# Performance work log

Measured on AMD Instinct MI355X. Metric: run time of the kernel, lower is better.

The kernel has to match this reference:

```python
import jax, jax.numpy as jnp
import numpy as np

N_NODES = 100000
N_EDGES = 1600000
N_GRAPHS = 256
F_NODE, F_EDGE, HID, OUT = 64, 16, 128, 128
BN_SCALE = 1.0 / np.sqrt(1.0 + 1e-5)  # BatchNorm eval with running mean 0, var 1


def setup_inputs() -> dict:
    key = jax.random.key(0)
    ks = iter(jax.random.split(key, 64))
    inp = {}
    inp["x"] = jax.random.normal(next(ks), (N_NODES, F_NODE), dtype=jnp.float32)
    inp["edge_attr"] = jax.random.normal(next(ks), (N_EDGES, F_EDGE), dtype=jnp.float32)
    inp["edge_index"] = jax.random.randint(next(ks), (2, N_EDGES), 0, N_NODES)
    inp["batch"] = jnp.sort(jax.random.randint(next(ks), (N_NODES,), 0, N_GRAPHS))

    def p(shape, scale):
        return (jax.random.normal(next(ks), shape, dtype=jnp.float32) * scale)

    in_dims = [F_NODE, HID, HID]
    for i, d in enumerate(in_dims):
        inp[f"el_w{i}"] = p((F_EDGE, d), F_EDGE ** -0.5)
        inp[f"el_b{i}"] = jnp.zeros((d,), jnp.float32)
        inp[f"c{i}_w1"] = p((d, HID), d ** -0.5)
        inp[f"c{i}_b1"] = jnp.zeros((HID,), jnp.float32)
        inp[f"c{i}_g"] = jnp.ones((HID,), jnp.float32)
        inp[f"c{i}_bt"] = jnp.zeros((HID,), jnp.float32)
        inp[f"c{i}_w2"] = p((HID, HID), HID ** -0.5)
        inp[f"c{i}_b2"] = jnp.zeros((HID,), jnp.float32)
    inp["o_w1"] = p((HID, OUT), HID ** -0.5)
    inp["o_b1"] = jnp.zeros((OUT,), jnp.float32)
    inp["o_w2"] = p((OUT, OUT), OUT ** -0.5)
    inp["o_b2"] = jnp.zeros((OUT,), jnp.float32)
    return inp


def reference(x, edge_attr,
              el_w0, el_b0, c0_w1, c0_b1, c0_g, c0_bt, c0_w2, c0_b2,
              el_w1, el_b1, c1_w1, c1_b1, c1_g, c1_bt, c1_w2, c1_b2,
              el_w2, el_b2, c2_w1, c2_b1, c2_g, c2_bt, c2_w2, c2_b2,
              o_w1, o_b1, o_w2, o_b2,
              edge_index, batch):
    src, dst = edge_index[0], edge_index[1]
    n = x.shape[0]
    layers = [
        (el_w0, el_b0, c0_w1, c0_b1, c0_g, c0_bt, c0_w2, c0_b2),
        (el_w1, el_b1, c1_w1, c1_b1, c1_g, c1_bt, c1_w2, c1_b2),
        (el_w2, el_b2, c2_w1, c2_b1, c2_g, c2_bt, c2_w2, c2_b2),
    ]
    h = x
    for (ew, eb, w1, b1, g, bt, w2, b2) in layers:
        ea = edge_attr @ ew + eb                              # [E, d]
        msg = jax.nn.relu(h[src] + ea)                        # GINEConv message
        agg = jax.ops.segment_sum(msg, dst, num_segments=n)   # scatter-sum to targets
        hh = h + agg                                          # (1+eps)*x + aggr, eps=0
        hh = hh @ w1 + b1                                     # MLP: Linear
        hh = g * (hh * BN_SCALE) + bt                         # BatchNorm1d (eval)
        hh = jax.nn.relu(hh)
        hh = hh @ w2 + b2                                     # MLP: Linear
        h = jax.nn.relu(hh)                                   # dropout(p=0, eval) + act
    s = jax.ops.segment_sum(h, batch, num_segments=N_GRAPHS)
    cnt = jax.ops.segment_sum(jnp.ones((n,), h.dtype), batch, num_segments=N_GRAPHS)
    pooled = s / jnp.maximum(cnt, 1.0)[:, None]               # scatter-mean pooling
    out = jax.nn.relu(pooled @ o_w1 + o_b1) @ o_w2 + o_b2     # out_lin
    return out
```

## Files before the change

### kernel.cpp

```cpp
#include <hip/hip_runtime.h>
#include <hip/hip_fp16.h>
#include <cstdint>
#include <cstddef>

#define N_NODES_C  100000
#define N_EDGES_C  1600000
#define N_GRAPHS_C 256
#define HID_C      128
#define BN_SCALE_C 0.9999950000374997f

#define SCAN_B 1024
#define SCAN_NB ((N_NODES_C + SCAN_B - 1) / SCAN_B)

typedef _Float16 h8 __attribute__((ext_vector_type(8)));
typedef _Float16 h4 __attribute__((ext_vector_type(4)));
typedef float    f4 __attribute__((ext_vector_type(4)));

struct __align__(16) H8 { __half2 v[4]; };
struct __align__(8)  Hq { __half2 a, b; };

__global__ __launch_bounds__(256) void hist_kernel(
    const int* __restrict__ dst, int* __restrict__ counts, int n_edges)
{
    int e = blockIdx.x * 256 + threadIdx.x;
    if (e < n_edges) atomicAdd(&counts[dst[e]], 1);
}

__global__ __launch_bounds__(SCAN_B) void scan1_kernel(
    const int* __restrict__ counts, int* __restrict__ incl,
    int* __restrict__ blocksums, int n)
{
    __shared__ int sdata[SCAN_B];
    const int lid = threadIdx.x;
    const int i = blockIdx.x * SCAN_B + lid;
    sdata[lid] = (i < n) ? counts[i] : 0;
    __syncthreads();
#pragma unroll
    for (int off = 1; off < SCAN_B; off <<= 1) {
        int t = (lid >= off) ? sdata[lid - off] : 0;
        __syncthreads();
        sdata[lid] += t;
        __syncthreads();
    }
    if (i < n) incl[i] = sdata[lid];
    if (lid == SCAN_B - 1) blocksums[blockIdx.x] = sdata[lid];
}

__global__ void scan2_kernel(const int* __restrict__ blocksums,
                             int* __restrict__ blockoffs, int nb)
{
    if (threadIdx.x == 0 && blockIdx.x == 0) {
        int off = 0;
        for (int b = 0; b < nb; ++b) { blockoffs[b] = off; off += blocksums[b]; }
    }
}

__global__ __launch_bounds__(SCAN_B) void scan3_kernel(
    int* __restrict__ incl, const int* __restrict__ blockoffs, int n)
{
    const int i = blockIdx.x * SCAN_B + threadIdx.x;
    if (i < n) incl[i] += blockoffs[blockIdx.x];
}

__global__ __launch_bounds__(256) void initrows_kernel(
    const int* __restrict__ incl, const int* __restrict__ counts,
    int* __restrict__ rowstart, int* __restrict__ cursor, int n)
{
    const int i = blockIdx.x * 256 + threadIdx.x;
    if (i < n) {
        const int rs = incl[i] - counts[i];
        rowstart[i] = rs;
        cursor[i]   = rs;
    }
}

__global__ __launch_bounds__(256) void scatter_kernel(
    const int* __restrict__ src, const int* __restrict__ dst,
    int* __restrict__ cursor, int* __restrict__ perm_src,
    int* __restrict__ perm_eid, int n_edges)
{
    const int e = blockIdx.x * 256 + threadIdx.x;
    if (e < n_edges) {
        const int pos = atomicAdd(&cursor[dst[e]], 1);
        perm_src[pos] = src[e];
        perm_eid[pos] = e;
    }
}

__global__ __launch_bounds__(256) void permute_ea_f16_kernel(
    const float* __restrict__ edge_attr, const int* __restrict__ perm_eid,
    __half* __restrict__ ea_f16, int n_edges)
{
    const int j = blockIdx.x * 256 + threadIdx.x;
    if (j >= n_edges) return;
    const int eid = perm_eid[j];
    const float4* p = (const float4*)(edge_attr + (size_t)eid * 16);
    const float4 q0 = p[0], q1 = p[1], q2 = p[2], q3 = p[3];
    H8 a, b;
    a.v[0] = __floats2half2_rn(q0.x, q0.y);
    a.v[1] = __floats2half2_rn(q0.z, q0.w);
    a.v[2] = __floats2half2_rn(q1.x, q1.y);
    a.v[3] = __floats2half2_rn(q1.z, q1.w);
    b.v[0] = __floats2half2_rn(q2.x, q2.y);
    b.v[1] = __floats2half2_rn(q2.z, q2.w);
    b.v[2] = __floats2half2_rn(q3.x, q3.y);
    b.v[3] = __floats2half2_rn(q3.z, q3.w);
    H8* o = (H8*)(ea_f16 + (size_t)j * 16);
    o[0] = a;
    o[1] = b;
}

__global__ __launch_bounds__(256) void cast_f16_kernel(
    const float* __restrict__ in, _Float16* __restrict__ out, int n4)
{
    const int i = blockIdx.x * 256 + threadIdx.x;
    if (i >= n4) return;
    const float4 v = ((const float4*)in)[i];
    h4 o; o[0] = (_Float16)v.x; o[1] = (_Float16)v.y;
    o[2] = (_Float16)v.z; o[3] = (_Float16)v.w;
    *(h4*)(out + (size_t)i * 4) = o;
}

__global__ __launch_bounds__(256) void transpose_w_kernel(
    const float* __restrict__ w, _Float16* __restrict__ wt, int K, int N)
{
    const int i = blockIdx.x * 256 + threadIdx.x;
    if (i >= K * N) return;
    const int n = i / K;
    const int k = i - n * K;
    wt[(size_t)n * K + k] = (_Float16)w[(size_t)k * N + n];
}

__device__ __forceinline__ float4 eamlp_f16(const H8* __restrict__ p,
                                            const __half2 (*ew2)[4],
                                            const float4 ebv)
{
    const H8 a = p[0], b = p[1];
    __half2 c0 = {0.f, 0.f}, c1 = {0.f, 0.f}, c2 = {0.f, 0.f}, c3 = {0.f, 0.f};
#pragma unroll
    for (int k2 = 0; k2 < 4; ++k2) {
        c0 = __hfma2(a.v[k2], ew2[k2][0], c0);
        c1 = __hfma2(a.v[k2], ew2[k2][1], c1);
        c2 = __hfma2(a.v[k2], ew2[k2][2], c2);
        c3 = __hfma2(a.v[k2], ew2[k2][3], c3);
    }
#pragma unroll
    for (int k2 = 0; k2 < 4; ++k2) {
        c0 = __hfma2(b.v[k2], ew2[4 + k2][0], c0);
        c1 = __hfma2(b.v[k2], ew2[4 + k2][1], c1);
        c2 = __hfma2(b.v[k2], ew2[4 + k2][2], c2);
        c3 = __hfma2(b.v[k2], ew2[4 + k2][3], c3);
    }
    float4 m;
    m.x = ebv.x + __low2float(c0) + __high2float(c0);
    m.y = ebv.y + __low2float(c1) + __high2float(c1);
    m.z = ebv.z + __low2float(c2) + __high2float(c2);
    m.w = ebv.w + __low2float(c3) + __high2float(c3);
    return m;
}

template<int DIN>
__global__ __launch_bounds__(256) void gine_agg_kernel(
    const __half* __restrict__ h16, const __half* __restrict__ ea_f16,
    const int* __restrict__ perm_src,
    const int* __restrict__ rowstart, const int* __restrict__ rowend,
    const float* __restrict__ ew, const float* __restrict__ eb,
    float* __restrict__ agg, int n_nodes)
{
    constexpr int NQ    = DIN / 4;
    constexpr int SLOTS = 256 / NQ;
    const int fq   = threadIdx.x & (NQ - 1);
    const int slot = threadIdx.x / NQ;
    const int v = blockIdx.x * SLOTS + slot;
    if (v >= n_nodes) return;

    __half2 ew2[8][4];
#pragma unroll
    for (int k2 = 0; k2 < 8; ++k2)
#pragma unroll
        for (int fi = 0; fi < 4; ++fi)
            ew2[k2][fi] = __floats2half2_rn(ew[(size_t)(2 * k2)     * DIN + fq * 4 + fi],
                                            ew[(size_t)(2 * k2 + 1) * DIN + fq * 4 + fi]);
    const float4 ebv = *(const float4*)(eb + fq * 4);

    const int s0 = rowstart[v];
    const int s1 = rowend[v];

    float4 acc = {0.f, 0.f, 0.f, 0.f};
    int j = s0;
    for (; j + 2 <= s1; j += 2) {
        const int sn0 = perm_src[j + 0];
        const int sn1 = perm_src[j + 1];
        const Hq hq0 = *(const Hq*)(h16 + (size_t)sn0 * DIN + fq * 4);
        const Hq hq1 = *(const Hq*)(h16 + (size_t)sn1 * DIN + fq * 4);
        const H8* p0 = (const H8*)(ea_f16 + (size_t)(j + 0) * 16);
        const H8* p1 = (const H8*)(ea_f16 + (size_t)(j + 1) * 16);
        const float4 m0 = eamlp_f16(p0, ew2, ebv);
        const float4 m1 = eamlp_f16(p1, ew2, ebv);
        const float2 l0 = __half22float2(hq0.a), u0 = __half22float2(hq0.b);
        const float2 l1 = __half22float2(hq1.a), u1 = __half22float2(hq1.b);
        acc.x += fmaxf(m0.x + l0.x, 0.f) + fmaxf(m1.x + l1.x, 0.f);
        acc.y += fmaxf(m0.y + l0.y, 0.f) + fmaxf(m1.y + l1.y, 0.f);
        acc.z += fmaxf(m0.z + u0.x, 0.f) + fmaxf(m1.z + u1.x, 0.f);
        acc.w += fmaxf(m0.w + u0.y, 0.f) + fmaxf(m1.w + u1.y, 0.f);
    }
    if (j < s1) {
        const int sn = perm_src[j];
        const Hq hq = *(const Hq*)(h16 + (size_t)sn * DIN + fq * 4);
        const H8* p = (const H8*)(ea_f16 + (size_t)j * 16);
        const float4 m = eamlp_f16(p, ew2, ebv);
        const float2 l = __half22float2(hq.a), u = __half22float2(hq.b);
        acc.x += fmaxf(m.x + l.x, 0.f);
        acc.y += fmaxf(m.y + l.y, 0.f);
        acc.z += fmaxf(m.z + u.x, 0.f);
        acc.w += fmaxf(m.w + u.y, 0.f);
    }
    *(float4*)(agg + (size_t)v * DIN + fq * 4) = acc;
}

template<int DIN>
__global__ __launch_bounds__(256) void node_mfma_kernel(
    const float* __restrict__ h, const float* __restrict__ agg,
    const _Float16* __restrict__ w1t, const float* __restrict__ b1,
    const float* __restrict__ gm, const float* __restrict__ bt,
    const _Float16* __restrict__ w2t, const float* __restrict__ b2,
    float* __restrict__ hout, _Float16* __restrict__ h16out, int n_tiles)
{
    constexpr int SXP = DIN + 8;
    constexpr int STP = HID_C + 8;
    __shared__ _Float16 s_x[4][16][SXP];
    __shared__ _Float16 s_t[4][16][STP];

    const int w    = threadIdx.x >> 6;
    const int lane = threadIdx.x & 63;
    int tile = blockIdx.x * 4 + w;
    if (tile >= n_tiles) tile = n_tiles - 1;
    const int node0 = tile * 16;

    constexpr int KQ = DIN / 4;
    for (int it = lane; it < 16 * KQ; it += 64) {
        const int ni = it / KQ;
        const int k4 = (it - ni * KQ) * 4;
        const float4 hv = *(const float4*)(h   + (size_t)(node0 + ni) * DIN + k4);
        const float4 av = *(const float4*)(agg + (size_t)(node0 + ni) * DIN + k4);
        h4 o;
        o[0] = (_Float16)(hv.x + av.x);
        o[1] = (_Float16)(hv.y + av.y);
        o[2] = (_Float16)(hv.z + av.z);
        o[3] = (_Float16)(hv.w + av.w);
        *(h4*)&s_x[w][ni][k4] = o;
    }
    __syncthreads();

    const int ln   = lane & 15;
    const int quad = lane >> 4;

#pragma unroll
    for (int nt = 0; nt < 8; ++nt) {
        const int col = nt * 16 + ln;
        const float bv = b1[col];
        f4 acc = {bv, bv, bv, bv};
#pragma unroll
        for (int ks = 0; ks < DIN / 32; ++ks) {
            const h8 af = *(const h8*)&s_x[w][ln][ks * 32 + quad * 8];
            const h8 bf = *(const h8*)(w1t + (size_t)col * DIN + ks * 32 + quad * 8);
            acc = __builtin_amdgcn_mfma_f32_16x16x32_f16(af, bf, acc, 0, 0, 0);
        }
        const float gv = gm[col], btv = bt[col];
#pragma unroll
        for (int r = 0; r < 4; ++r) {
            const float t = fmaxf(fmaf(acc[r] * BN_SCALE_C, gv, btv), 0.f);
            s_t[w][quad * 4 + r][col] = (_Float16)t;
        }
    }
    __syncthreads();

#pragma unroll
    for (int nt = 0; nt < 8; ++nt) {
        const int col = nt * 16 + ln;
        const float bv = b2[col];
        f4 acc = {bv, bv, bv, bv};
#pragma unroll
        for (int ks = 0; ks < HID_C / 32; ++ks) {
            const h8 af = *(const h8*)&s_t[w][ln][ks * 32 + quad * 8];
            const h8 bf = *(const h8*)(w2t + (size_t)col * HID_C + ks * 32 + quad * 8);
            acc = __builtin_amdgcn_mfma_f32_16x16x32_f16(af, bf, acc, 0, 0, 0);
        }
#pragma unroll
        for (int r = 0; r < 4; ++r) {
            const int node = node0 + quad * 4 + r;
            const float v = fmaxf(acc[r], 0.f);
            hout[(size_t)node * HID_C + col] = v;
            h16out[(size_t)node * HID_C + col] = (_Float16)v;
        }
    }
}

__global__ __launch_bounds__(256) void pool_kernel(
    const float* __restrict__ hfin, const int* __restrict__ batch,
    const float* __restrict__ w1, const float* __restrict__ b1,
    const float* __restrict__ w2, const float* __restrict__ b2,
    float* __restrict__ out, int n_nodes)
{
    const int gid = blockIdx.x;

    int lo = 0, hi = n_nodes;
    while (lo < hi) { int mid = (lo + hi) >> 1; if (batch[mid] < gid) lo = mid + 1; else hi = mid; }
    const int start = lo;
    hi = n_nodes;
    while (lo < hi) { int mid = (lo + hi) >> 1; if (batch[mid] < gid + 1) lo = mid + 1; else hi = mid; }
    const int end = lo;

    const int f = threadIdx.x & (HID_C - 1);
    const int half = threadIdx.x >> 7;

    float sum = 0.f;
    for (int n = start + half; n < end; n += 2)
        sum += hfin[(size_t)n * HID_C + f];

    __shared__ float s_sum[2][HID_C];
    __shared__ float s_p[HID_C];
    __shared__ float s_t[HID_C];
    s_sum[half][f] = sum;
    __syncthreads();

    if (threadIdx.x < HID_C) {
        const float cnt = (float)(end - start);
        s_p[f] = (s_sum[0][f] + s_sum[1][f]) / fmaxf(cnt, 1.f);
    }
    __syncthreads();

    if (threadIdx.x < HID_C) {
        float acc = b1[f];
        for (int k = 0; k < HID_C; ++k) acc = fmaf(s_p[k], w1[k * HID_C + f], acc);
        s_t[f] = fmaxf(acc, 0.f);
    }
    __syncthreads();

    if (threadIdx.x < HID_C) {
        float acc = b2[f];
        for (int k = 0; k < HID_C; ++k) acc = fmaf(s_t[k], w2[k * HID_C + f], acc);
        out[(size_t)gid * HID_C + f] = acc;
    }
}

extern "C" void kernel_launch(void* const* d_in, const int* in_sizes, int n_in,
                              void* d_out, int out_size, void* d_ws, size_t ws_size,
                              hipStream_t stream)
{
    const float* x         = (const float*)d_in[0];
    const float* edge_attr = (const float*)d_in[1];
    const int*   edge_index= (const int*)  d_in[2];
    const int*   batch     = (const int*)  d_in[3];
    const int*   src = edge_index;
    const int*   dst = edge_index + N_EDGES_C;

    const float* el_w[3] = {(const float*)d_in[4],  (const float*)d_in[12], (const float*)d_in[20]};
    const float* el_b[3] = {(const float*)d_in[5],  (const float*)d_in[13], (const float*)d_in[21]};
    const float* c_w1[3] = {(const float*)d_in[6],  (const float*)d_in[14], (const float*)d_in[22]};
    const float* c_b1[3] = {(const float*)d_in[7],  (const float*)d_in[15], (const float*)d_in[23]};
    const float* c_g [3] = {(const float*)d_in[8],  (const float*)d_in[16], (const float*)d_in[24]};
    const float* c_bt[3] = {(const float*)d_in[9],  (const float*)d_in[17], (const float*)d_in[25]};
    const float* c_w2[3] = {(const float*)d_in[10], (const float*)d_in[18], (const float*)d_in[26]};
    const float* c_b2[3] = {(const float*)d_in[11], (const float*)d_in[19], (const float*)d_in[27]};
    const float* o_w1 = (const float*)d_in[28];
    const float* o_b1 = (const float*)d_in[29];
    const float* o_w2 = (const float*)d_in[30];
    const float* o_b2 = (const float*)d_in[31];

    char* wsp = (char*)d_ws;
    size_t used = 0;
    auto alloc = [&](size_t bytes) { char* p = wsp + used; used += (bytes + 255) & ~(size_t)255; return p; };
    float* h        = (float*)alloc((size_t)N_NODES_C * HID_C * 4);
    float* agg      = (float*)alloc((size_t)N_NODES_C * HID_C * 4);
    int*   counts   = (int*)alloc((size_t)N_NODES_C * 4);
    int*   incl     = (int*)alloc((size_t)N_NODES_C * 4);
    int*   rowstart = (int*)alloc((size_t)N_NODES_C * 4);
    int*   cursor   = (int*)alloc((size_t)N_NODES_C * 4);
    int*   blocksums= (int*)alloc(128 * 4);
    int*   blockoffs= (int*)alloc(128 * 4);
    int*   perm_src = (int*)alloc((size_t)N_EDGES_C * 4);
    int*   perm_eid = (int*)alloc((size_t)N_EDGES_C * 4);
    __half*    ea_f16 = (__half*)alloc((size_t)N_EDGES_C * 16 * 2);
    _Float16*  h_f16  = (_Float16*)alloc((size_t)N_NODES_C * HID_C * 2);
    _Float16*  x_f16  = (_Float16*)alloc((size_t)N_NODES_C * 64 * 2);
    _Float16*  w1t[3], *w2t[3];
    for (int l = 0; l < 3; ++l) {
        w1t[l] = (_Float16*)alloc((size_t)HID_C * HID_C * 2);
        w2t[l] = (_Float16*)alloc((size_t)HID_C * HID_C * 2);
    }
    (void)ws_size;

    hipMemsetAsync(counts, 0, (size_t)N_NODES_C * 4, stream);
    hist_kernel<<<(N_EDGES_C + 255) / 256, 256, 0, stream>>>(dst, counts, N_EDGES_C);
    scan1_kernel<<<SCAN_NB, SCAN_B, 0, stream>>>(counts, incl, blocksums, N_NODES_C);
    scan2_kernel<<<1, 64, 0, stream>>>(blocksums, blockoffs, SCAN_NB);
    scan3_kernel<<<SCAN_NB, SCAN_B, 0, stream>>>(incl, blockoffs, N_NODES_C);
    initrows_kernel<<<(N_NODES_C + 255) / 256, 256, 0, stream>>>(incl, counts, rowstart,
                                                                 cursor, N_NODES_C);
    scatter_kernel<<<(N_EDGES_C + 255) / 256, 256, 0, stream>>>(src, dst, cursor,
                                                                perm_src, perm_eid, N_EDGES_C);
    permute_ea_f16_kernel<<<(N_EDGES_C + 255) / 256, 256, 0, stream>>>(
        edge_attr, perm_eid, ea_f16, N_EDGES_C);
    cast_f16_kernel<<<(N_NODES_C * 64 / 4 + 255) / 256, 256, 0, stream>>>(
        x, x_f16, N_NODES_C * 64 / 4);
    for (int l = 0; l < 3; ++l) {
        const int K1 = (l == 0) ? 64 : HID_C;
        transpose_w_kernel<<<(K1 * HID_C + 255) / 256, 256, 0, stream>>>(
            c_w1[l], w1t[l], K1, HID_C);
        transpose_w_kernel<<<(HID_C * HID_C + 255) / 256, 256, 0, stream>>>(
            c_w2[l], w2t[l], HID_C, HID_C);
    }

    const int n_tiles = N_NODES_C / 16;
    const int nb_node = (n_tiles + 3) / 4;

    for (int l = 0; l < 3; ++l) {
        if (l == 0) {
            gine_agg_kernel<64><<<(N_NODES_C + 15) / 16, 256, 0, stream>>>(
                (const __half*)x_f16, ea_f16, perm_src, rowstart, incl,
                el_w[0], el_b[0], agg, N_NODES_C);
            node_mfma_kernel<64><<<nb_node, 256, 0, stream>>>(
                x, agg, w1t[0], c_b1[0], c_g[0], c_bt[0], w2t[0], c_b2[0],
                h, h_f16, n_tiles);
        } else {
            gine_agg_kernel<128><<<(N_NODES_C + 7) / 8, 256, 0, stream>>>(
                (const __half*)h_f16, ea_f16, perm_src, rowstart, incl,
                el_w[l], el_b[l], agg, N_NODES_C);
            node_mfma_kernel<128><<<nb_node, 256, 0, stream>>>(
                h, agg, w1t[l], c_b1[l], c_g[l], c_bt[l], w2t[l], c_b2[l],
                h, h_f16, n_tiles);
        }
    }

    pool_kernel<<<N_GRAPHS_C, 256, 0, stream>>>(h, batch, o_w1, o_b1, o_w2, o_b2,
                                                (float*)d_out, N_NODES_C);
}
```

Before: 1.114 ms.

## Fuse edge aggregation with node MLP into one per-layer kernel

Merges the gather/aggregate kernel and the MFMA node MLP kernel into a single per-layer kernel. Each wavefront aggregates messages for its 16-node tile straight into shared memory, which removes the fp32 agg buffer round trip and the fp32 h reads. Hidden states now ping-pong between fp16 buffers, and only the last layer writes fp32. The edge MLP switches from packed half FMAs to fdot2 with fp32 accumulation. Blocks shrink to 128 threads with 2 tiles each, which may cost load balance and repeats the edge-weight register setup per wave.

```diff
diff --git a/kernel.cpp b/kernel.cpp
--- a/kernel.cpp
+++ b/kernel.cpp
@@ -12,12 +12,32 @@
 #define SCAN_B 1024
 #define SCAN_NB ((N_NODES_C + SCAN_B - 1) / SCAN_B)
 
+typedef _Float16 h2 __attribute__((ext_vector_type(2)));
+typedef _Float16 h4 __attribute__((ext_vector_type(4)));
 typedef _Float16 h8 __attribute__((ext_vector_type(8)));
-typedef _Float16 h4 __attribute__((ext_vector_type(4)));
 typedef float    f4 __attribute__((ext_vector_type(4)));
 
+struct __align__(16) EA8 { h2 p[4]; };
+struct __align__(8)  HQ  { h2 a, b; };
 struct __align__(16) H8 { __half2 v[4]; };
-struct __align__(8)  Hq { __half2 a, b; };
+
+#if defined(__has_builtin)
+#  if __has_builtin(__builtin_amdgcn_fdot2)
+#    define HAVE_FDOT2 1
+#  endif
+#endif
+#ifndef HAVE_FDOT2
+#  define HAVE_FDOT2 0
+#endif
+
+__device__ __forceinline__ float fdot2_(h2 a, h2 b, float c)
+{
+#if HAVE_FDOT2
+    return __builtin_amdgcn_fdot2(a, b, c, false);
+#else
+    return c + (float)a[0] * (float)b[0] + (float)a[1] * (float)b[1];
+#endif
+}
 
 __global__ __launch_bounds__(256) void hist_kernel(
     const int* __restrict__ dst, int* __restrict__ counts, int n_edges)
@@ -131,96 +151,13 @@
     wt[(size_t)n * K + k] = (_Float16)w[(size_t)k * N + n];
 }
 
-__device__ __forceinline__ float4 eamlp_f16(const H8* __restrict__ p,
-                                            const __half2 (*ew2)[4],
-                                            const float4 ebv)
-{
-    const H8 a = p[0], b = p[1];
-    __half2 c0 = {0.f, 0.f}, c1 = {0.f, 0.f}, c2 = {0.f, 0.f}, c3 = {0.f, 0.f};
-#pragma unroll
-    for (int k2 = 0; k2 < 4; ++k2) {
-        c0 = __hfma2(a.v[k2], ew2[k2][0], c0);
-        c1 = __hfma2(a.v[k2], ew2[k2][1], c1);
-        c2 = __hfma2(a.v[k2], ew2[k2][2], c2);
-        c3 = __hfma2(a.v[k2], ew2[k2][3], c3);
-    }
-#pragma unroll
-    for (int k2 = 0; k2 < 4; ++k2) {
-        c0 = __hfma2(b.v[k2], ew2[4 + k2][0], c0);
-        c1 = __hfma2(b.v[k2], ew2[4 + k2][1], c1);
-        c2 = __hfma2(b.v[k2], ew2[4 + k2][2], c2);
-        c3 = __hfma2(b.v[k2], ew2[4 + k2][3], c3);
-    }
-    float4 m;
-    m.x = ebv.x + __low2float(c0) + __high2float(c0);
-    m.y = ebv.y + __low2float(c1) + __high2float(c1);
-    m.z = ebv.z + __low2float(c2) + __high2float(c2);
-    m.w = ebv.w + __low2float(c3) + __high2float(c3);
-    return m;
-}
-
-template<int DIN>
-__global__ __launch_bounds__(256) void gine_agg_kernel(
-    const __half* __restrict__ h16, const __half* __restrict__ ea_f16,
+template<int DIN, bool LASTL>
+__global__ __launch_bounds__(128) void gine_layer_kernel(
+    const _Float16* __restrict__ hin,
+    const _Float16* __restrict__ ea16,
     const int* __restrict__ perm_src,
     const int* __restrict__ rowstart, const int* __restrict__ rowend,
     const float* __restrict__ ew, const float* __restrict__ eb,
-    float* __restrict__ agg, int n_nodes)
-{
-    constexpr int NQ    = DIN / 4;
-    constexpr int SLOTS = 256 / NQ;
-    const int fq   = threadIdx.x & (NQ - 1);
-    const int slot = threadIdx.x / NQ;
-    const int v = blockIdx.x * SLOTS + slot;
-    if (v >= n_nodes) return;
-
-    __half2 ew2[8][4];
-#pragma unroll
-    for (int k2 = 0; k2 < 8; ++k2)
-#pragma unroll
-        for (int fi = 0; fi < 4; ++fi)
-            ew2[k2][fi] = __floats2half2_rn(ew[(size_t)(2 * k2)     * DIN + fq * 4 + fi],
-                                            ew[(size_t)(2 * k2 + 1) * DIN + fq * 4 + fi]);
-    const float4 ebv = *(const float4*)(eb + fq * 4);
-
-    const int s0 = rowstart[v];
-    const int s1 = rowend[v];
-
-    float4 acc = {0.f, 0.f, 0.f, 0.f};
-    int j = s0;
-    for (; j + 2 <= s1; j += 2) {
-        const int sn0 = perm_src[j + 0];
-        const int sn1 = perm_src[j + 1];
-        const Hq hq0 = *(const Hq*)(h16 + (size_t)sn0 * DIN + fq * 4);
-        const Hq hq1 = *(const Hq*)(h16 + (size_t)sn1 * DIN + fq * 4);
-        const H8* p0 = (const H8*)(ea_f16 + (size_t)(j + 0) * 16);
-        const H8* p1 = (const H8*)(ea_f16 + (size_t)(j + 1) * 16);
-        const float4 m0 = eamlp_f16(p0, ew2, ebv);
-        const float4 m1 = eamlp_f16(p1, ew2, ebv);
-        const float2 l0 = __half22float2(hq0.a), u0 = __half22float2(hq0.b);
-        const float2 l1 = __half22float2(hq1.a), u1 = __half22float2(hq1.b);
-        acc.x += fmaxf(m0.x + l0.x, 0.f) + fmaxf(m1.x + l1.x, 0.f);
-        acc.y += fmaxf(m0.y + l0.y, 0.f) + fmaxf(m1.y + l1.y, 0.f);
-        acc.z += fmaxf(m0.z + u0.x, 0.f) + fmaxf(m1.z + u1.x, 0.f);
-        acc.w += fmaxf(m0.w + u0.y, 0.f) + fmaxf(m1.w + u1.y, 0.f);
-    }
-    if (j < s1) {
-        const int sn = perm_src[j];
-        const Hq hq = *(const Hq*)(h16 + (size_t)sn * DIN + fq * 4);
-        const H8* p = (const H8*)(ea_f16 + (size_t)j * 16);
-        const float4 m = eamlp_f16(p, ew2, ebv);
-        const float2 l = __half22float2(hq.a), u = __half22float2(hq.b);
-        acc.x += fmaxf(m.x + l.x, 0.f);
-        acc.y += fmaxf(m.y + l.y, 0.f);
-        acc.z += fmaxf(m.z + u.x, 0.f);
-        acc.w += fmaxf(m.w + u.y, 0.f);
-    }
-    *(float4*)(agg + (size_t)v * DIN + fq * 4) = acc;
-}
-
-template<int DIN>
-__global__ __launch_bounds__(256) void node_mfma_kernel(
-    const float* __restrict__ h, const float* __restrict__ agg,
     const _Float16* __restrict__ w1t, const float* __restrict__ b1,
     const float* __restrict__ gm, const float* __restrict__ bt,
     const _Float16* __restrict__ w2t, const float* __restrict__ b2,
@@ -228,27 +165,111 @@
 {
     constexpr int SXP = DIN + 8;
     constexpr int STP = HID_C + 8;
-    __shared__ _Float16 s_x[4][16][SXP];
-    __shared__ _Float16 s_t[4][16][STP];
+    __shared__ _Float16 s_x[2][16][SXP];
+    __shared__ _Float16 s_t[2][16][STP];
 
     const int w    = threadIdx.x >> 6;
     const int lane = threadIdx.x & 63;
-    int tile = blockIdx.x * 4 + w;
+    int tile = blockIdx.x * 2 + w;
     if (tile >= n_tiles) tile = n_tiles - 1;
     const int node0 = tile * 16;
 
-    constexpr int KQ = DIN / 4;
-    for (int it = lane; it < 16 * KQ; it += 64) {
-        const int ni = it / KQ;
-        const int k4 = (it - ni * KQ) * 4;
-        const float4 hv = *(const float4*)(h   + (size_t)(node0 + ni) * DIN + k4);
-        const float4 av = *(const float4*)(agg + (size_t)(node0 + ni) * DIN + k4);
+    constexpr int NQ  = DIN / 4;
+    constexpr int GPW = 64 / NQ;
+    constexpr int NPG = 16 / GPW;
+    const int fq = lane & (NQ - 1);
+    const int g  = lane / NQ;
+
+    h2 ew2h[8][4];
+#pragma unroll
+    for (int k2 = 0; k2 < 8; ++k2)
+#pragma unroll
+        for (int fi = 0; fi < 4; ++fi) {
+            h2 t;
+            t[0] = (_Float16)ew[(size_t)(2 * k2)     * DIN + fq * 4 + fi];
+            t[1] = (_Float16)ew[(size_t)(2 * k2 + 1) * DIN + fq * 4 + fi];
+            ew2h[k2][fi] = t;
+        }
+    const float4 ebv = *(const float4*)(eb + fq * 4);
+
+#pragma unroll
+    for (int i = 0; i < NPG; ++i) {
+        const int ni = g * NPG + i;
+        const int v  = node0 + ni;
+        const int s0 = rowstart[v];
+        const int s1 = rowend[v];
+
+        float4 acc = {0.f, 0.f, 0.f, 0.f};
+        int j = s0;
+        for (; j + 2 <= s1; j += 2) {
+            const int sn0 = perm_src[j + 0];
+            const int sn1 = perm_src[j + 1];
+            const HQ hq0 = *(const HQ*)(hin + (size_t)sn0 * DIN + fq * 4);
+            const HQ hq1 = *(const HQ*)(hin + (size_t)sn1 * DIN + fq * 4);
+            const EA8* pe = (const EA8*)(ea16 + (size_t)j * 16);
+            const EA8 a0 = pe[0], c0 = pe[1], a1 = pe[2], c1 = pe[3];
+            float4 m0 = {ebv.x, ebv.y, ebv.z, ebv.w};
+            float4 m1 = m0;
+#pragma unroll
+            for (int k = 0; k < 4; ++k) {
+                m0.x = fdot2_(a0.p[k], ew2h[k][0], m0.x);
+                m0.y = fdot2_(a0.p[k], ew2h[k][1], m0.y);
+                m0.z = fdot2_(a0.p[k], ew2h[k][2], m0.z);
+                m0.w = fdot2_(a0.p[k], ew2h[k][3], m0.w);
+                m1.x = fdot2_(a1.p[k], ew2h[k][0], m1.x);
+                m1.y = fdot2_(a1.p[k], ew2h[k][1], m1.y);
+                m1.z = fdot2_(a1.p[k], ew2h[k][2], m1.z);
+                m1.w = fdot2_(a1.p[k], ew2h[k][3], m1.w);
+            }
+#pragma unroll
+            for (int k = 0; k < 4; ++k) {
+                m0.x = fdot2_(c0.p[k], ew2h[4 + k][0], m0.x);
+                m0.y = fdot2_(c0.p[k], ew2h[4 + k][1], m0.y);
+                m0.z = fdot2_(c0.p[k], ew2h[4 + k][2], m0.z);
+                m0.w = fdot2_(c0.p[k], ew2h[4 + k][3], m0.w);
+                m1.x = fdot2_(c1.p[k], ew2h[4 + k][0], m1.x);
+                m1.y = fdot2_(c1.p[k], ew2h[4 + k][1], m1.y);
+                m1.z = fdot2_(c1.p[k], ew2h[4 + k][2], m1.z);
+                m1.w = fdot2_(c1.p[k], ew2h[4 + k][3], m1.w);
+            }
+            acc.x += fmaxf(m0.x + (float)hq0.a[0], 0.f) + fmaxf(m1.x + (float)hq1.a[0], 0.f);
+            acc.y += fmaxf(m0.y + (float)hq0.a[1], 0.f) + fmaxf(m1.y + (float)hq1.a[1], 0.f);
+            acc.z += fmaxf(m0.z + (float)hq0.b[0], 0.f) + fmaxf(m1.z + (float)hq1.b[0], 0.f);
+            acc.w += fmaxf(m0.w + (float)hq0.b[1], 0.f) + fmaxf(m1.w + (float)hq1.b[1], 0.f);
+        }
+        if (j < s1) {
+            const int sn = perm_src[j];
+            const HQ hq = *(const HQ*)(hin + (size_t)sn * DIN + fq * 4);
+            const EA8* pe = (const EA8*)(ea16 + (size_t)j * 16);
+            const EA8 a0 = pe[0], c0 = pe[1];
+            float4 m0 = {ebv.x, ebv.y, ebv.z, ebv.w};
+#pragma unroll
+            for (int k = 0; k < 4; ++k) {
+                m0.x = fdot2_(a0.p[k], ew2h[k][0], m0.x);
+                m0.y = fdot2_(a0.p[k], ew2h[k][1], m0.y);
+                m0.z = fdot2_(a0.p[k], ew2h[k][2], m0.z);
+                m0.w = fdot2_(a0.p[k], ew2h[k][3], m0.w);
+            }
+#pragma unroll
+            for (int k = 0; k < 4; ++k) {
+                m0.x = fdot2_(c0.p[k], ew2h[4 + k][0], m0.x);
+                m0.y = fdot2_(c0.p[k], ew2h[4 + k][1], m0.y);
+                m0.z = fdot2_(c0.p[k], ew2h[4 + k][2], m0.z);
+                m0.w = fdot2_(c0.p[k], ew2h[4 + k][3], m0.w);
+            }
+            acc.x += fmaxf(m0.x + (float)hq.a[0], 0.f);
+            acc.y += fmaxf(m0.y + (float)hq.a[1], 0.f);
+            acc.z += fmaxf(m0.z + (float)hq.b[0], 0.f);
+            acc.w += fmaxf(m0.w + (float)hq.b[1], 0.f);
+        }
+
+        const HQ hv = *(const HQ*)(hin + (size_t)v * DIN + fq * 4);
         h4 o;
-        o[0] = (_Float16)(hv.x + av.x);
-        o[1] = (_Float16)(hv.y + av.y);
-        o[2] = (_Float16)(hv.z + av.z);
-        o[3] = (_Float16)(hv.w + av.w);
-        *(h4*)&s_x[w][ni][k4] = o;
+        o[0] = (_Float16)(acc.x + (float)hv.a[0]);
+        o[1] = (_Float16)(acc.y + (float)hv.a[1]);
+        o[2] = (_Float16)(acc.z + (float)hv.b[0]);
+        o[3] = (_Float16)(acc.w + (float)hv.b[1]);
+        *(h4*)&s_x[w][ni][fq * 4] = o;
     }
     __syncthreads();
 
@@ -290,8 +311,11 @@
         for (int r = 0; r < 4; ++r) {
             const int node = node0 + quad * 4 + r;
             const float v = fmaxf(acc[r], 0.f);
-            hout[(size_t)node * HID_C + col] = v;
-            h16out[(size_t)node * HID_C + col] = (_Float16)v;
+            if (LASTL) {
+                hout[(size_t)node * HID_C + col] = v;
+            } else {
+                h16out[(size_t)node * HID_C + col] = (_Float16)v;
+            }
         }
     }
 }
@@ -372,7 +396,6 @@
     size_t used = 0;
     auto alloc = [&](size_t bytes) { char* p = wsp + used; used += (bytes + 255) & ~(size_t)255; return p; };
     float* h        = (float*)alloc((size_t)N_NODES_C * HID_C * 4);
-    float* agg      = (float*)alloc((size_t)N_NODES_C * HID_C * 4);
     int*   counts   = (int*)alloc((size_t)N_NODES_C * 4);
     int*   incl     = (int*)alloc((size_t)N_NODES_C * 4);
     int*   rowstart = (int*)alloc((size_t)N_NODES_C * 4);
@@ -381,10 +404,11 @@
     int*   blockoffs= (int*)alloc(128 * 4);
     int*   perm_src = (int*)alloc((size_t)N_EDGES_C * 4);
     int*   perm_eid = (int*)alloc((size_t)N_EDGES_C * 4);
-    __half*    ea_f16 = (__half*)alloc((size_t)N_EDGES_C * 16 * 2);
-    _Float16*  h_f16  = (_Float16*)alloc((size_t)N_NODES_C * HID_C * 2);
-    _Float16*  x_f16  = (_Float16*)alloc((size_t)N_NODES_C * 64 * 2);
-    _Float16*  w1t[3], *w2t[3];
+    _Float16* ea_f16 = (_Float16*)alloc((size_t)N_EDGES_C * 16 * 2);
+    _Float16* h16_a  = (_Float16*)alloc((size_t)N_NODES_C * HID_C * 2);
+    _Float16* h16_b  = (_Float16*)alloc((size_t)N_NODES_C * HID_C * 2);
+    _Float16* x_f16  = (_Float16*)alloc((size_t)N_NODES_C * 64 * 2);
+    _Float16* w1t[3], *w2t[3];
     for (int l = 0; l < 3; ++l) {
         w1t[l] = (_Float16*)alloc((size_t)HID_C * HID_C * 2);
         w2t[l] = (_Float16*)alloc((size_t)HID_C * HID_C * 2);
@@ -401,7 +425,7 @@
     scatter_kernel<<<(N_EDGES_C + 255) / 256, 256, 0, stream>>>(src, dst, cursor,
                                                                 perm_src, perm_eid, N_EDGES_C);
     permute_ea_f16_kernel<<<(N_EDGES_C + 255) / 256, 256, 0, stream>>>(
-        edge_attr, perm_eid, ea_f16, N_EDGES_C);
+        edge_attr, perm_eid, (__half*)ea_f16, N_EDGES_C);
     cast_f16_kernel<<<(N_NODES_C * 64 / 4 + 255) / 256, 256, 0, stream>>>(
         x, x_f16, N_NODES_C * 64 / 4);
     for (int l = 0; l < 3; ++l) {
@@ -413,25 +437,20 @@
     }
 
     const int n_tiles = N_NODES_C / 16;
-    const int nb_node = (n_tiles + 3) / 4;
-
-    for (int l = 0; l < 3; ++l) {
-        if (l == 0) {
-            gine_agg_kernel<64><<<(N_NODES_C + 15) / 16, 256, 0, stream>>>(
-                (const __half*)x_f16, ea_f16, perm_src, rowstart, incl,
-                el_w[0], el_b[0], agg, N_NODES_C);
-            node_mfma_kernel<64><<<nb_node, 256, 0, stream>>>(
-                x, agg, w1t[0], c_b1[0], c_g[0], c_bt[0], w2t[0], c_b2[0],
-                h, h_f16, n_tiles);
-        } else {
-            gine_agg_kernel<128><<<(N_NODES_C + 7) / 8, 256, 0, stream>>>(
-                (const __half*)h_f16, ea_f16, perm_src, rowstart, incl,
-                el_w[l], el_b[l], agg, N_NODES_C);
-            node_mfma_kernel<128><<<nb_node, 256, 0, stream>>>(
-                h, agg, w1t[l], c_b1[l], c_g[l], c_bt[l], w2t[l], c_b2[l],
-                h, h_f16, n_tiles);
-        }
-    }
+    const int nb = (n_tiles + 1) / 2;
+
+    gine_layer_kernel<64, false><<<nb, 128, 0, stream>>>(
+        x_f16, ea_f16, perm_src, rowstart, incl,
+        el_w[0], el_b[0], w1t[0], c_b1[0], c_g[0], c_bt[0], w2t[0], c_b2[0],
+        h, h16_a, n_tiles);
+    gine_layer_kernel<128, false><<<nb, 128, 0, stream>>>(
+        h16_a, ea_f16, perm_src, rowstart, incl,
+        el_w[1], el_b[1], w1t[1], c_b1[1], c_g[1], c_bt[1], w2t[1], c_b2[1],
+        h, h16_b, n_tiles);
+    gine_layer_kernel<128, true><<<nb, 128, 0, stream>>>(
+        h16_b, ea_f16, perm_src, rowstart, incl,
+        el_w[2], el_b[2], w1t[2], c_b1[2], c_g[2], c_bt[2], w2t[2], c_b2[2],
+        h, h16_a, n_tiles);
 
     pool_kernel<<<N_GRAPHS_C, 256, 0, stream>>>(h, batch, o_w1, o_b1, o_w2, o_b2,
                                                 (float*)d_out, N_NODES_C);
```

Result: faster. 1.048 ms (-5.9%).
